# Kernel optimization log

Hardware: AMD Instinct MI355X
Metric: run time of the kernel (lower is better)

The kernel has to match this reference:

```python
import jax, jax.numpy as jnp
import numpy as np

N_NODES = 100000
D_IN = 128
D_OUT = 128
B, T, S = 8, 4096, 25


def setup_inputs() -> dict:
    key = jax.random.key(0)
    k1, k2, k3 = jax.random.split(key, 3)
    features = jax.random.normal(k1, (N_NODES, D_IN), dtype=jnp.float32)
    sample_res = jax.random.randint(k2, (B, T, S), 0, N_NODES, dtype=jnp.int64)
    # glorot-uniform init for [D_IN, D_OUT]
    limit = np.sqrt(6.0 / (D_IN + D_OUT)).astype(np.float32)
    weights = jax.random.uniform(k3, (D_IN, D_OUT), dtype=jnp.float32,
                                 minval=-limit, maxval=limit)
    return {"features": features, "sample_res": sample_res, "weights": weights}


def reference(features, sample_res, weights):
    # gather neighbor embeddings: [B, T, S, D]
    sampled = features[sample_res]
    # mean over sampled-neighbor axis -> [B, T, D]
    neigh_vecs = jnp.mean(sampled, axis=2)
    # shared linear transform + relu (bias=False per init defaults)
    out = jnp.einsum('btd,do->bto', neigh_vecs, weights)
    return jax.nn.relu(out)
```

## Files before the change

kernel.cpp:

```cpp
#include <hip/hip_runtime.h>


#define DEG 25
#define DIM 128
#define RPB 16
#define BLOCK 256
#define CG 32

__device__ __forceinline__ float4 relu4(float4 v) {
    return make_float4(fmaxf(v.x, 0.f), fmaxf(v.y, 0.f),
                       fmaxf(v.z, 0.f), fmaxf(v.w, 0.f));
}

__global__ __launch_bounds__(BLOCK, 4) void gcn_fused(
    const float* __restrict__ F,
    const int*   __restrict__ idx,
    const float* __restrict__ W,
    float*       __restrict__ out,
    int n_rows)
{
    __shared__ float4 sV[RPB * CG];
    __shared__ int    sIdx[RPB * DEG];

    const float4* F4   = (const float4*)F;
    const float4* W4   = (const float4*)W;
    float4*       out4 = (float4*)out;

    const int tid  = threadIdx.x;
    const int row0 = blockIdx.x * RPB;

    for (int i = tid; i < RPB * DEG; i += BLOCK)
        sIdx[i] = idx[(size_t)row0 * DEG + i];
    __syncthreads();

    const int cg = tid & 31;
    const int rs = tid >> 5;

#pragma unroll
    for (int rr = 0; rr < 2; ++rr) {
        const int r = rs + rr * 8;
        int j[DEG];
#pragma unroll
        for (int s = 0; s < DEG; ++s) j[s] = sIdx[r * DEG + s];
        float4 acc = make_float4(0.f, 0.f, 0.f, 0.f);
#pragma unroll
        for (int s = 0; s < DEG; ++s) {
            float4 f = F4[(size_t)j[s] * CG + cg];
            acc.x += f.x; acc.y += f.y; acc.z += f.z; acc.w += f.w;
        }
        const float inv = 1.0f / 25.0f;
        acc.x *= inv; acc.y *= inv; acc.z *= inv; acc.w *= inv;
        sV[r * CG + cg] = acc;
    }
    __syncthreads();

    const float4* vA = &sV[rs * CG];
    const float4* vB = &sV[(rs + 8) * CG];
    float4 o0 = make_float4(0.f, 0.f, 0.f, 0.f);
    float4 o1 = make_float4(0.f, 0.f, 0.f, 0.f);
#pragma unroll 4
    for (int d4 = 0; d4 < CG; ++d4) {
        const float4 a = vA[d4];
        const float4 b = vB[d4];
        const float4 w0 = W4[(size_t)(4 * d4 + 0) * CG + cg];
        const float4 w1 = W4[(size_t)(4 * d4 + 1) * CG + cg];
        const float4 w2 = W4[(size_t)(4 * d4 + 2) * CG + cg];
        const float4 w3 = W4[(size_t)(4 * d4 + 3) * CG + cg];

        o0.x += a.x * w0.x; o0.y += a.x * w0.y; o0.z += a.x * w0.z; o0.w += a.x * w0.w;
        o0.x += a.y * w1.x; o0.y += a.y * w1.y; o0.z += a.y * w1.z; o0.w += a.y * w1.w;
        o0.x += a.z * w2.x; o0.y += a.z * w2.y; o0.z += a.z * w2.z; o0.w += a.z * w2.w;
        o0.x += a.w * w3.x; o0.y += a.w * w3.y; o0.z += a.w * w3.z; o0.w += a.w * w3.w;

        o1.x += b.x * w0.x; o1.y += b.x * w0.y; o1.z += b.x * w0.z; o1.w += b.x * w0.w;
        o1.x += b.y * w1.x; o1.y += b.y * w1.y; o1.z += b.y * w1.z; o1.w += b.y * w1.w;
        o1.x += b.z * w2.x; o1.y += b.z * w2.y; o1.z += b.z * w2.z; o1.w += b.z * w2.w;
        o1.x += b.w * w3.x; o1.y += b.w * w3.y; o1.z += b.w * w3.z; o1.w += b.w * w3.w;
    }

    out4[(size_t)(row0 + rs) * CG + cg]     = relu4(o0);
    out4[(size_t)(row0 + rs + 8) * CG + cg] = relu4(o1);
}

extern "C" void kernel_launch(void* const* d_in, const int* in_sizes, int n_in,
                              void* d_out, int out_size, void* d_ws, size_t ws_size,
                              hipStream_t stream) {
    const float* F   = (const float*)d_in[0];
    const int*   idx = (const int*)d_in[1];
    const float* W   = (const float*)d_in[2];
    float* out = (float*)d_out;

    const int n_rows = in_sizes[1] / DEG;
    const int grid = n_rows / RPB;
    gcn_fused<<<grid, BLOCK, 0, stream>>>(F, idx, W, out, n_rows);
}
```

Baseline: 143.2 us.

## Transform all node features with a bf16 MFMA GEMM, then gather-mean the results

Measured after the change: 133.9 us. 1.07x faster.

```diff
diff --git a/kernel.cpp b/kernel.cpp
--- a/kernel.cpp
+++ b/kernel.cpp
@@ -3,8 +3,157 @@
 
 #define DEG 25
 #define DIM 128
+
+typedef __attribute__((ext_vector_type(8))) short short8;
+typedef __attribute__((ext_vector_type(4))) float floatx4;
+
+__device__ __forceinline__ unsigned short f2bf(float f) {
+    unsigned u = __float_as_uint(f);
+    return (unsigned short)((u + 0x7fffu + ((u >> 16) & 1u)) >> 16);
+}
+
+#define BSTRIDE 136
+
+__global__ __launch_bounds__(256, 2) void gemm_fw(
+    const float* __restrict__ A,
+    const float* __restrict__ B,
+    unsigned short* __restrict__ G,
+    int M)
+{
+    __shared__ unsigned short sBt[DIM * BSTRIDE];
+
+    const int tid = threadIdx.x;
+
+    {
+        const float4* B4 = (const float4*)B;
+#pragma unroll
+        for (int i = 0; i < 16; ++i) {
+            const int linear = i * 256 + tid;
+            const int k  = linear >> 5;
+            const int c4 = linear & 31;
+            const float4 v = B4[linear];
+            const int n = c4 * 4;
+            sBt[(n + 0) * BSTRIDE + k] = f2bf(v.x);
+            sBt[(n + 1) * BSTRIDE + k] = f2bf(v.y);
+            sBt[(n + 2) * BSTRIDE + k] = f2bf(v.z);
+            sBt[(n + 3) * BSTRIDE + k] = f2bf(v.w);
+        }
+    }
+    __syncthreads();
+
+    const int wave = tid >> 6;
+    const int lane = tid & 63;
+    const int quad = lane >> 4;
+    const int l16  = lane & 15;
+
+    const int rw0 = blockIdx.x * 128 + wave * 32;
+
+    floatx4 acc[2][8];
+#pragma unroll
+    for (int mt = 0; mt < 2; ++mt)
+#pragma unroll
+        for (int nt = 0; nt < 8; ++nt)
+            acc[mt][nt] = (floatx4){0.f, 0.f, 0.f, 0.f};
+
+#pragma unroll
+    for (int kt = 0; kt < 4; ++kt) {
+        const int k0 = kt * 32;
+
+        short8 afrag[2];
+#pragma unroll
+        for (int mt = 0; mt < 2; ++mt) {
+            int row = rw0 + mt * 16 + l16;
+            if (row >= M) row = M - 1;
+            const float* ap = A + (size_t)row * DIM + k0 + quad * 8;
+            const float4 x = *(const float4*)ap;
+            const float4 y = *(const float4*)(ap + 4);
+            unsigned p0 = (unsigned)f2bf(x.x) | ((unsigned)f2bf(x.y) << 16);
+            unsigned p1 = (unsigned)f2bf(x.z) | ((unsigned)f2bf(x.w) << 16);
+            unsigned p2 = (unsigned)f2bf(y.x) | ((unsigned)f2bf(y.y) << 16);
+            unsigned p3 = (unsigned)f2bf(y.z) | ((unsigned)f2bf(y.w) << 16);
+            uint4 packed = make_uint4(p0, p1, p2, p3);
+            afrag[mt] = __builtin_bit_cast(short8, packed);
+        }
+
+#pragma unroll
+        for (int nt = 0; nt < 8; ++nt) {
+            const uint4 u = *(const uint4*)&sBt[(nt * 16 + l16) * BSTRIDE + k0 + quad * 8];
+            const short8 bfrag = __builtin_bit_cast(short8, u);
+#pragma unroll
+            for (int mt = 0; mt < 2; ++mt)
+                acc[mt][nt] = __builtin_amdgcn_mfma_f32_16x16x32_bf16(
+                    afrag[mt], bfrag, acc[mt][nt], 0, 0, 0);
+        }
+    }
+
+#pragma unroll
+    for (int mt = 0; mt < 2; ++mt)
+#pragma unroll
+        for (int nt = 0; nt < 8; ++nt)
+#pragma unroll
+            for (int r = 0; r < 4; ++r) {
+                const int row = rw0 + mt * 16 + quad * 4 + r;
+                if (row < M)
+                    G[(size_t)row * DIM + nt * 16 + l16] = f2bf(acc[mt][nt][r]);
+            }
+}
+
+#define GRPB 32
+
+__global__ __launch_bounds__(256, 4) void gather_mean_relu(
+    const unsigned short* __restrict__ G,
+    const int* __restrict__ idx,
+    float* __restrict__ out,
+    int n_rows)
+{
+    __shared__ int sIdx[GRPB * DEG];
+
+    const int tid  = threadIdx.x;
+    const int row0 = blockIdx.x * GRPB;
+
+    for (int i = tid; i < GRPB * DEG; i += 256)
+        sIdx[i] = idx[(size_t)row0 * DEG + i];
+    __syncthreads();
+
+    const int grp = tid >> 4;
+    const int l16 = tid & 15;
+    const uint4* G4 = (const uint4*)G;
+    float4* out4 = (float4*)out;
+
+#pragma unroll
+    for (int rr = 0; rr < 2; ++rr) {
+        const int r = grp + rr * 16;
+
+        uint4 v[DEG];
+#pragma unroll
+        for (int s = 0; s < DEG; ++s)
+            v[s] = G4[(size_t)sIdx[r * DEG + s] * 16 + l16];
+
+        float a0 = 0.f, a1 = 0.f, a2 = 0.f, a3 = 0.f;
+        float a4 = 0.f, a5 = 0.f, a6 = 0.f, a7 = 0.f;
+#pragma unroll
+        for (int s = 0; s < DEG; ++s) {
+            a0 += __uint_as_float(v[s].x << 16);
+            a1 += __uint_as_float(v[s].x & 0xffff0000u);
+            a2 += __uint_as_float(v[s].y << 16);
+            a3 += __uint_as_float(v[s].y & 0xffff0000u);
+            a4 += __uint_as_float(v[s].z << 16);
+            a5 += __uint_as_float(v[s].z & 0xffff0000u);
+            a6 += __uint_as_float(v[s].w << 16);
+            a7 += __uint_as_float(v[s].w & 0xffff0000u);
+        }
+        const float inv = 1.0f / 25.0f;
+        float4 o0 = make_float4(fmaxf(a0 * inv, 0.f), fmaxf(a1 * inv, 0.f),
+                                fmaxf(a2 * inv, 0.f), fmaxf(a3 * inv, 0.f));
+        float4 o1 = make_float4(fmaxf(a4 * inv, 0.f), fmaxf(a5 * inv, 0.f),
+                                fmaxf(a6 * inv, 0.f), fmaxf(a7 * inv, 0.f));
+        const size_t ob = (size_t)(row0 + r) * 32 + l16 * 2;
+        out4[ob]     = o0;
+        out4[ob + 1] = o1;
+    }
+}
+
 #define RPB 16
-#define BLOCK 256
 #define CG 32
 
 __device__ __forceinline__ float4 relu4(float4 v) {
@@ -12,24 +161,21 @@
                        fmaxf(v.z, 0.f), fmaxf(v.w, 0.f));
 }
 
-__global__ __launch_bounds__(BLOCK, 4) void gcn_fused(
-    const float* __restrict__ F,
-    const int*   __restrict__ idx,
-    const float* __restrict__ W,
-    float*       __restrict__ out,
-    int n_rows)
+__global__ __launch_bounds__(256, 4) void gcn_fused(
+    const float* __restrict__ F, const int* __restrict__ idx,
+    const float* __restrict__ W, float* __restrict__ out, int n_rows)
 {
     __shared__ float4 sV[RPB * CG];
     __shared__ int    sIdx[RPB * DEG];
 
-    const float4* F4   = (const float4*)F;
-    const float4* W4   = (const float4*)W;
-    float4*       out4 = (float4*)out;
-
-    const int tid  = threadIdx.x;
+    const float4* F4 = (const float4*)F;
+    const float4* W4 = (const float4*)W;
+    float4* out4 = (float4*)out;
+
+    const int tid = threadIdx.x;
     const int row0 = blockIdx.x * RPB;
 
-    for (int i = tid; i < RPB * DEG; i += BLOCK)
+    for (int i = tid; i < RPB * DEG; i += 256)
         sIdx[i] = idx[(size_t)row0 * DEG + i];
     __syncthreads();
 
@@ -55,7 +201,7 @@
     __syncthreads();
 
     const float4* vA = &sV[rs * CG];
-    const float4* vB = &sV[(rs + 8) * CG];
+    const float4* vB = vA + DIM / 4 * 0 + 8 * CG;
     float4 o0 = make_float4(0.f, 0.f, 0.f, 0.f);
     float4 o1 = make_float4(0.f, 0.f, 0.f, 0.f);
 #pragma unroll 4
@@ -66,18 +212,15 @@
         const float4 w1 = W4[(size_t)(4 * d4 + 1) * CG + cg];
         const float4 w2 = W4[(size_t)(4 * d4 + 2) * CG + cg];
         const float4 w3 = W4[(size_t)(4 * d4 + 3) * CG + cg];
-
-        o0.x += a.x * w0.x; o0.y += a.x * w0.y; o0.z += a.x * w0.z; o0.w += a.x * w0.w;
-        o0.x += a.y * w1.x; o0.y += a.y * w1.y; o0.z += a.y * w1.z; o0.w += a.y * w1.w;
-        o0.x += a.z * w2.x; o0.y += a.z * w2.y; o0.z += a.z * w2.z; o0.w += a.z * w2.w;
-        o0.x += a.w * w3.x; o0.y += a.w * w3.y; o0.z += a.w * w3.z; o0.w += a.w * w3.w;
-
-        o1.x += b.x * w0.x; o1.y += b.x * w0.y; o1.z += b.x * w0.z; o1.w += b.x * w0.w;
-        o1.x += b.y * w1.x; o1.y += b.y * w1.y; o1.z += b.y * w1.z; o1.w += b.y * w1.w;
-        o1.x += b.z * w2.x; o1.y += b.z * w2.y; o1.z += b.z * w2.z; o1.w += b.z * w2.w;
-        o1.x += b.w * w3.x; o1.y += b.w * w3.y; o1.z += b.w * w3.z; o1.w += b.w * w3.w;
-    }
-
+        o0.x += a.x*w0.x + a.y*w1.x + a.z*w2.x + a.w*w3.x;
+        o0.y += a.x*w0.y + a.y*w1.y + a.z*w2.y + a.w*w3.y;
+        o0.z += a.x*w0.z + a.y*w1.z + a.z*w2.z + a.w*w3.z;
+        o0.w += a.x*w0.w + a.y*w1.w + a.z*w2.w + a.w*w3.w;
+        o1.x += b.x*w0.x + b.y*w1.x + b.z*w2.x + b.w*w3.x;
+        o1.y += b.x*w0.y + b.y*w1.y + b.z*w2.y + b.w*w3.y;
+        o1.z += b.x*w0.z + b.y*w1.z + b.z*w2.z + b.w*w3.z;
+        o1.w += b.x*w0.w + b.y*w1.w + b.z*w2.w + b.w*w3.w;
+    }
     out4[(size_t)(row0 + rs) * CG + cg]     = relu4(o0);
     out4[(size_t)(row0 + rs + 8) * CG + cg] = relu4(o1);
 }
@@ -90,7 +233,15 @@
     const float* W   = (const float*)d_in[2];
     float* out = (float*)d_out;
 
-    const int n_rows = in_sizes[1] / DEG;
-    const int grid = n_rows / RPB;
-    gcn_fused<<<grid, BLOCK, 0, stream>>>(F, idx, W, out, n_rows);
-}
+    const int n_nodes = in_sizes[0] / DIM;
+    const int n_rows  = in_sizes[1] / DEG;
+
+    const size_t need = (size_t)n_nodes * DIM * sizeof(unsigned short);
+    if (ws_size >= need) {
+        unsigned short* G = (unsigned short*)d_ws;
+        gemm_fw<<<(n_nodes + 127) / 128, 256, 0, stream>>>(F, W, G, n_nodes);
+        gather_mean_relu<<<n_rows / GRPB, 256, 0, stream>>>(G, idx, out, n_rows);
+    } else {
+        gcn_fused<<<n_rows / RPB, 256, 0, stream>>>(F, idx, W, out, n_rows);
+    }
+}
```
